# Kernel tuning notes

Measured on AMD Instinct MI355X. Metric: run time of the kernel, lower is better.

The kernel has to match this reference:

```python
import jax, jax.numpy as jnp
import numpy as np

EPS = 1e-6

def _ln(x):
    mu = jnp.mean(x, -1, keepdims=True)
    var = jnp.mean((x - mu) ** 2, -1, keepdims=True)
    return (x - mu) / jnp.sqrt(var + EPS)

def _mha(q_in, k_in, v_in, w, mask, h):
    # w: [4, d, d] = (Wq, Wk, Wv, Wo), stored as [in, out]
    b, sq, d = q_in.shape
    dk = d // h
    q = (q_in @ w[0]).reshape(b, sq, h, dk)
    k = (k_in @ w[1]).reshape(b, k_in.shape[1], h, dk)
    v = (v_in @ w[2]).reshape(b, v_in.shape[1], h, dk)
    scores = jnp.einsum('bqhd,bkhd->bhqk', q, k) / np.sqrt(dk).astype(q.dtype)
    if mask is not None:
        scores = jnp.where(mask, scores, jnp.asarray(-jnp.inf, scores.dtype))
    attn = jax.nn.softmax(scores, -1)
    out = jnp.einsum('bhqk,bkhd->bqhd', attn, v).reshape(b, sq, d)
    return out @ w[3]

def setup_inputs() -> dict:
    B, S, D, V, NL, ML = 8, 256, 1024, 32000, 6, 256
    ks = jax.random.split(jax.random.key(0), 8)
    sc = 0.02
    return {
        'memory': jax.random.normal(ks[0], (B, S, D), jnp.float32),
        'gold_tokens': jax.random.randint(ks[1], (B, ML), 0, V),
        'attn_w': jax.random.normal(ks[2], (NL, 2, 4, D, D), jnp.float32) * sc,
        'ffn_w1': jax.random.normal(ks[3], (NL, D, 4 * D), jnp.float32) * sc,
        'ffn_w2': jax.random.normal(ks[4], (NL, 4 * D, D), jnp.float32) * sc,
        'tok_emb': jax.random.normal(ks[5], (V, D - ML), jnp.float32) * sc,
        'sos': jax.random.normal(ks[6], (D,), jnp.float32),
        'gen_w': jax.random.normal(ks[7], (D, V), jnp.float32) * sc,
    }

def reference(memory, gold_tokens, attn_w, ffn_w1, ffn_w2, tok_emb, sos, gen_w):
    B = memory.shape[0]
    ML = gold_tokens.shape[1]          # max_length == decoder len
    NL = attn_w.shape[0]
    H = 8
    temperature = 1.0
    # embedding: token embed (dim d-ML) concat one-hot position (dim ML)
    dec_input = gold_tokens[:, :-1]                      # [B, ML-1]
    tok = tok_emb[dec_input]                             # [B, ML-1, D-ML]
    pos = jax.nn.one_hot(jnp.arange(ML - 1), ML, dtype=tok.dtype)  # [ML-1, ML]
    pos = jnp.broadcast_to(pos[None], (B, ML - 1, ML))
    emb = jnp.concatenate([tok, pos], -1)                # [B, ML-1, D]
    sos_tok = jnp.broadcast_to(sos[None, None, :], (B, 1, sos.shape[0]))
    x = jnp.concatenate([sos_tok, emb], 1)               # [B, ML, D]
    causal = jnp.tril(jnp.ones((ML, ML), bool))[None, None]  # True = keep
    for l in range(NL):
        h1 = _ln(x)
        x = x + _mha(h1, h1, h1, attn_w[l, 0], causal, H)       # self-attn
        x = x + _mha(_ln(x), memory, memory, attn_w[l, 1], None, H)  # cross-attn (raw memory keys/values)
        h2 = _ln(x)
        x = x + jax.nn.relu(h2 @ ffn_w1[l]) @ ffn_w2[l]
    logits = _ln(x) @ gen_w
    return jax.nn.log_softmax(logits / temperature, -1)
```

## Files before the change

kernel.cpp:

```cpp
#include <hip/hip_runtime.h>
#include <hip/hip_bf16.h>
#include <cstdint>
#include <cstddef>

using bf16 = __hip_bfloat16;
typedef __attribute__((ext_vector_type(8))) short bf16x8;
typedef __attribute__((ext_vector_type(4))) float f32x4;

#define DEV static __device__ __forceinline__

DEV unsigned short f2bf(float f) {
    bf16 h = __float2bfloat16(f);
    return __builtin_bit_cast(unsigned short, h);
}

typedef const __attribute__((address_space(1))) void* as1cv;
typedef __attribute__((address_space(3))) void* as3v;

DEV void load_lds16(const void* g, void* l) {
    __builtin_amdgcn_global_load_lds((as1cv)g, (as3v)l, 16, 0, 0);
}

template<int EPI>
__global__ __launch_bounds__(256)
void gemm_k(const bf16* __restrict__ Ag, const bf16* __restrict__ Bg,
            void* __restrict__ Cg,
            int Mdim, int Ndim, int Kdim,
            int lda, int ldb, int ldc,
            int Hdim, long aZ1, long aZ2, long bZ1, long bZ2,
            long cZ1, long cZ2, float scale,
            const bf16* __restrict__ Ag2, int ySplitA)
{
    __shared__ __align__(16) char lds[65536];

    const int t = threadIdx.x;
    const int wave = t >> 6, lane = t & 63;
    const int wr = wave >> 1, wc = wave & 1;
    const int lo = lane & 15, hi = lane >> 4;

    const int bx2 = blockIdx.x, by2 = blockIdx.y;
    const int m0 = bx2 * 128, n0 = by2 * 128;
    const int z = blockIdx.z;
    const int z1 = z / Hdim, z2 = z - z1 * Hdim;

    const bf16* Abase = (by2 >= ySplitA) ? Ag2 : Ag;
    const bf16* A = Abase + (size_t)z1 * aZ1 + (size_t)z2 * aZ2;
    const bf16* B = Bg + (size_t)z1 * bZ1 + (size_t)z2 * bZ2;

    f32x4 acc[4][4];
#pragma unroll
    for (int m = 0; m < 4; ++m)
#pragma unroll
        for (int n = 0; n < 4; ++n)
            acc[m][n] = f32x4{0.f, 0.f, 0.f, 0.f};

    const int nk = Kdim >> 6;

    auto stage = [&](int kt, int buf) {
        const int k0 = kt << 6;
        char* dA = lds + buf * 32768;
        char* dB = dA + 16384;
#pragma unroll
        for (int i = 0; i < 4; ++i) {
            int u = i * 256 + t;
            int row = u >> 3;
            int cb = (u & 7) ^ (row & 7);
            load_lds16(A + (size_t)(m0 + row) * lda + (k0 + cb * 8),
                       dA + i * 4096 + wave * 1024);
        }
#pragma unroll
        for (int i = 0; i < 4; ++i) {
            int u = i * 256 + t;
            int row = u >> 3;
            int cb = (u & 7) ^ (row & 7);
            load_lds16(B + (size_t)(n0 + row) * ldb + (k0 + cb * 8),
                       dB + i * 4096 + wave * 1024);
        }
    };

    stage(0, 0);
    int cur = 0;
    for (int kt = 0; kt < nk; ++kt) {
        __syncthreads();
        if (kt + 1 < nk) stage(kt + 1, cur ^ 1);
        char* ldsA = lds + cur * 32768;
        char* ldsB = ldsA + 16384;
#pragma unroll
        for (int kk = 0; kk < 2; ++kk) {
            bf16x8 af[4], bfr[4];
#pragma unroll
            for (int m = 0; m < 4; ++m) {
                int row = wr * 64 + m * 16 + lo;
                int cbyte = ((kk << 6) + (hi << 4)) ^ ((row & 7) << 4);
                af[m] = *(const bf16x8*)(ldsA + row * 128 + cbyte);
            }
#pragma unroll
            for (int n = 0; n < 4; ++n) {
                int row = wc * 64 + n * 16 + lo;
                int cbyte = ((kk << 6) + (hi << 4)) ^ ((row & 7) << 4);
                bfr[n] = *(const bf16x8*)(ldsB + row * 128 + cbyte);
            }
#pragma unroll
            for (int m = 0; m < 4; ++m)
#pragma unroll
                for (int n = 0; n < 4; ++n)
                    acc[m][n] = __builtin_amdgcn_mfma_f32_16x16x32_bf16(
                        af[m], bfr[n], acc[m][n], 0, 0, 0);
        }
        cur ^= 1;
    }

    const int rb = hi << 2;
    if (EPI == 0 || EPI == 1) {
        unsigned short* C = (unsigned short*)Cg + (size_t)z1 * cZ1 + (size_t)z2 * cZ2;
#pragma unroll
        for (int m = 0; m < 4; ++m)
#pragma unroll
            for (int n = 0; n < 4; ++n)
#pragma unroll
                for (int r = 0; r < 4; ++r) {
                    int row = m0 + wr * 64 + m * 16 + rb + r;
                    int col = n0 + wc * 64 + n * 16 + lo;
                    float v = acc[m][n][r];
                    if (EPI == 1) v = fmaxf(v, 0.f);
                    C[(size_t)row * ldc + col] = f2bf(v);
                }
    } else if (EPI == 5) {
        float* C = (float*)Cg + (size_t)z1 * cZ1 + (size_t)z2 * cZ2;
#pragma unroll
        for (int m = 0; m < 4; ++m)
#pragma unroll
            for (int n = 0; n < 4; ++n)
#pragma unroll
                for (int r = 0; r < 4; ++r) {
                    int row = m0 + wr * 64 + m * 16 + rb + r;
                    int col = n0 + wc * 64 + n * 16 + lo;
                    atomicAdd(&C[(size_t)row * ldc + col], acc[m][n][r]);
                }
    } else {
        float* C = (float*)Cg + (size_t)z1 * cZ1 + (size_t)z2 * cZ2;
#pragma unroll
        for (int m = 0; m < 4; ++m)
#pragma unroll
            for (int n = 0; n < 4; ++n)
#pragma unroll
                for (int r = 0; r < 4; ++r) {
                    int row = m0 + wr * 64 + m * 16 + rb + r;
                    int col = n0 + wc * 64 + n * 16 + lo;
                    __builtin_nontemporal_store(acc[m][n][r] * scale,
                                                &C[(size_t)row * ldc + col]);
                }
    }
}

template<int CAUSAL>
__global__ __launch_bounds__(256)
void attn_k(const bf16* __restrict__ qkv, const bf16* __restrict__ VT,
            bf16* __restrict__ attno)
{
    __shared__ __align__(16) char ldsK[2][16384];
    __shared__ __align__(16) char ldsP[8192];
    const float SC = 0.088388347648318447f;

    const int t = threadIdx.x, w = t >> 6, lane = t & 63;
    const int lo = lane & 15, hi = lane >> 4;
    const int qb = blockIdx.x, z = blockIdx.y;
    const int b = z >> 3, h = z & 7;
    const int qr0 = qb * 64 + w * 16;

    const unsigned short* Qg = (const unsigned short*)qkv + (size_t)(b * 256) * 3072 + h * 128;
    const unsigned short* Kg = Qg + 1024;
    const unsigned short* VTz = (const unsigned short*)VT + (size_t)z * 32768;

    bf16x8 qf[4];
#pragma unroll
    for (int ks = 0; ks < 4; ++ks)
        qf[ks] = *(const bf16x8*)(Qg + (size_t)(qr0 + lo) * 3072 + ks * 32 + hi * 8);

    f32x4 accO[8];
#pragma unroll
    for (int n2 = 0; n2 < 8; ++n2) accO[n2] = f32x4{0.f, 0.f, 0.f, 0.f};
    float mrun[4], lrun[4];
#pragma unroll
    for (int r = 0; r < 4; ++r) { mrun[r] = -3.0e38f; lrun[r] = 0.f; }

    auto stageK = [&](int kt, int buf) {
#pragma unroll
        for (int i = 0; i < 4; ++i) {
            int u = i * 256 + t;
            int row = u >> 4, j = u & 15;
            int sj = (j & 8) | ((j ^ row) & 7);
            load_lds16(Kg + (size_t)(kt * 64 + row) * 3072 + sj * 8,
                       ldsK[buf] + i * 4096 + w * 1024);
        }
    };

    const int nkt = CAUSAL ? (qb + 1) : 4;
    stageK(0, 0);
    int cur = 0;
    for (int kt = 0; kt < nkt; ++kt) {
        __syncthreads();
        if (kt + 1 < nkt) stageK(kt + 1, cur ^ 1);

        f32x4 s4[4];
#pragma unroll
        for (int n = 0; n < 4; ++n) s4[n] = f32x4{0.f, 0.f, 0.f, 0.f};
#pragma unroll
        for (int ks = 0; ks < 4; ++ks)
#pragma unroll
            for (int n = 0; n < 4; ++n) {
                int kr = n * 16 + lo;
                int c = ks * 4 + hi;
                int sc2 = (c & 8) | ((c ^ (kr & 7)) & 7);
                bf16x8 kf = *(const bf16x8*)(ldsK[cur] + kr * 256 + sc2 * 16);
                s4[n] = __builtin_amdgcn_mfma_f32_16x16x32_bf16(qf[ks], kf, s4[n], 0, 0, 0);
            }

        float sv[4][4];
#pragma unroll
        for (int n = 0; n < 4; ++n)
#pragma unroll
            for (int r = 0; r < 4; ++r) {
                float v = s4[n][r] * SC;
                if (CAUSAL) {
                    int kg = kt * 64 + n * 16 + lo;
                    int qg2 = qb * 64 + w * 16 + hi * 4 + r;
                    if (kg > qg2) v = -3.0e38f;
                }
                sv[n][r] = v;
            }

        float sfv[4];
#pragma unroll
        for (int r = 0; r < 4; ++r) {
            float m2 = fmaxf(fmaxf(sv[0][r], sv[1][r]), fmaxf(sv[2][r], sv[3][r]));
#pragma unroll
            for (int o = 1; o < 16; o <<= 1) m2 = fmaxf(m2, __shfl_xor(m2, o));
            float mn = fmaxf(mrun[r], m2);
            sfv[r] = __expf(mrun[r] - mn);
            mrun[r] = mn;
        }
        float p[4][4], ts[4];
#pragma unroll
        for (int r = 0; r < 4; ++r) ts[r] = 0.f;
#pragma unroll
        for (int n = 0; n < 4; ++n)
#pragma unroll
            for (int r = 0; r < 4; ++r) {
                float e = __expf(sv[n][r] - mrun[r]);
                p[n][r] = e; ts[r] += e;
            }
#pragma unroll
        for (int r = 0; r < 4; ++r) {
            float s2 = ts[r];
#pragma unroll
            for (int o = 1; o < 16; o <<= 1) s2 += __shfl_xor(s2, o);
            lrun[r] = lrun[r] * sfv[r] + s2;
        }
#pragma unroll
        for (int n2 = 0; n2 < 8; ++n2)
#pragma unroll
            for (int r = 0; r < 4; ++r) accO[n2][r] *= sfv[r];

        char* pb = ldsP + w * 2048;
#pragma unroll
        for (int n = 0; n < 4; ++n)
#pragma unroll
            for (int r = 0; r < 4; ++r) {
                int q = hi * 4 + r, k = n * 16 + lo;
                int ch = (k >> 3) ^ (q & 7);
                *(unsigned short*)(pb + q * 128 + ch * 16 + (k & 7) * 2) = f2bf(p[n][r]);
            }

#pragma unroll
        for (int ks2 = 0; ks2 < 2; ++ks2) {
            int c2 = (ks2 * 4 + hi) ^ (lo & 7);
            bf16x8 pa = *(const bf16x8*)(pb + lo * 128 + c2 * 16);
#pragma unroll
            for (int n2 = 0; n2 < 8; ++n2) {
                int d = n2 * 16 + lo;
                bf16x8 vb = *(const bf16x8*)(VTz + (size_t)d * 256 + kt * 64 + ks2 * 32 + hi * 8);
                accO[n2] = __builtin_amdgcn_mfma_f32_16x16x32_bf16(pa, vb, accO[n2], 0, 0, 0);
            }
        }
        cur ^= 1;
    }

    float inv[4];
#pragma unroll
    for (int r = 0; r < 4; ++r) inv[r] = 1.f / lrun[r];
    unsigned short* Og = (unsigned short*)attno;
#pragma unroll
    for (int n2 = 0; n2 < 8; ++n2)
#pragma unroll
        for (int r = 0; r < 4; ++r) {
            int qg2 = qb * 64 + w * 16 + hi * 4 + r;
            int d = n2 * 16 + lo;
            Og[(size_t)(b * 256 + qg2) * 1024 + h * 128 + d] = f2bf(accO[n2][r] * inv[r]);
        }
}

DEV void wconv_tile(const float* __restrict__ W, unsigned short* __restrict__ WT,
                    int K, int N, int k0, int n0, int t, unsigned short* lds)
{
#pragma unroll
    for (int i = 0; i < 16; ++i) {
        int lin = i * 256 + t;
        int r = lin >> 6, c = lin & 63;
        float v = __builtin_nontemporal_load(&W[(size_t)(k0 + r) * N + n0 + c]);
        lds[c * 65 + r] = f2bf(v);
    }
    __syncthreads();
#pragma unroll
    for (int i = 0; i < 16; ++i) {
        int lin = i * 256 + t;
        int r = lin >> 6, c = lin & 63;
        WT[(size_t)(n0 + r) * K + k0 + c] = lds[r * 65 + c];
    }
}

__global__ __launch_bounds__(256)
void wconv_k(const float* __restrict__ W, bf16* __restrict__ WT, int K, int N)
{
    __shared__ unsigned short lds[64 * 65];
    size_t moff = (size_t)blockIdx.z * K * N;
    wconv_tile(W + moff, (unsigned short*)WT + moff, K, N,
               blockIdx.x * 64, blockIdx.y * 64, threadIdx.x, lds);
}

__global__ __launch_bounds__(256)
void wconv3_k(const float* __restrict__ Wa, const float* __restrict__ W1,
              const float* __restrict__ W2, bf16* __restrict__ WTa,
              bf16* __restrict__ WT1, bf16* __restrict__ WT2)
{
    __shared__ unsigned short lds[64 * 65];
    int bid = blockIdx.x, t = threadIdx.x;
    if (bid < 2048) {
        int mat = bid >> 8, r = bid & 255;
        size_t moff = (size_t)mat * 1048576;
        wconv_tile(Wa + moff, (unsigned short*)WTa + moff, 1024, 1024,
                   (r & 15) * 64, (r >> 4) * 64, t, lds);
    } else if (bid < 3072) {
        int idx = bid - 2048;
        wconv_tile(W1, (unsigned short*)WT1, 1024, 4096,
                   (idx & 15) * 64, (idx >> 4) * 64, t, lds);
    } else {
        int idx = bid - 3072;
        wconv_tile(W2, (unsigned short*)WT2, 4096, 1024,
                   (idx & 63) * 64, (idx >> 6) * 64, t, lds);
    }
}

__global__ __launch_bounds__(256)
void f2b_k(const float* __restrict__ in, bf16* __restrict__ out, int n4)
{
    int i = blockIdx.x * 256 + threadIdx.x;
    if (i >= n4) return;
    float4 v = ((const float4*)in)[i];
    ushort4 o;
    o.x = f2bf(v.x); o.y = f2bf(v.y); o.z = f2bf(v.z); o.w = f2bf(v.w);
    ((ushort4*)out)[i] = o;
}

__global__ __launch_bounds__(256)
void embed_k(const float* __restrict__ tok_emb, const int* __restrict__ gold,
             const float* __restrict__ sos, float* __restrict__ x)
{
    int row = blockIdx.x;
    int b = row >> 8, sq = row & 255;
    int c4 = threadIdx.x;
    float4 v;
    if (sq == 0) {
        v = ((const float4*)sos)[c4];
    } else {
        int c = c4 << 2;
        if (c < 768) {
            int tok = gold[b * 256 + sq - 1];
            v = ((const float4*)(tok_emb + (size_t)tok * 768))[c4];
        } else {
            int p = sq - 1;
            v.x = (c + 0 - 768 == p) ? 1.f : 0.f;
            v.y = (c + 1 - 768 == p) ? 1.f : 0.f;
            v.z = (c + 2 - 768 == p) ? 1.f : 0.f;
            v.w = (c + 3 - 768 == p) ? 1.f : 0.f;
        }
    }
    ((float4*)(x + (size_t)row * 1024))[c4] = v;
}

__global__ __launch_bounds__(256)
void ln_k(const float* __restrict__ x, bf16* __restrict__ out)
{
    int row = blockIdx.x;
    const float4* xr = (const float4*)(x + (size_t)row * 1024);
    float4 v = xr[threadIdx.x];
    float s = v.x + v.y + v.z + v.w;
    float ss = v.x * v.x + v.y * v.y + v.z * v.z + v.w * v.w;
    for (int o = 32; o > 0; o >>= 1) { s += __shfl_down(s, o); ss += __shfl_down(ss, o); }
    __shared__ float buf[8];
    int wv = threadIdx.x >> 6;
    if ((threadIdx.x & 63) == 0) { buf[wv] = s; buf[4 + wv] = ss; }
    __syncthreads();
    float S = buf[0] + buf[1] + buf[2] + buf[3];
    float SS = buf[4] + buf[5] + buf[6] + buf[7];
    float mean = S * (1.f / 1024.f);
    float var = SS * (1.f / 1024.f) - mean * mean;
    float rstd = rsqrtf(var + 1e-6f);
    ushort4 o;
    o.x = f2bf((v.x - mean) * rstd);
    o.y = f2bf((v.y - mean) * rstd);
    o.z = f2bf((v.z - mean) * rstd);
    o.w = f2bf((v.w - mean) * rstd);
    ((ushort4*)out)[(size_t)row * 256 + threadIdx.x] = o;
}

__global__ __launch_bounds__(256)
void vtrans_k(const bf16* __restrict__ v, bf16* __restrict__ VT)
{
    __shared__ unsigned short lds[128 * 65];
    int z = blockIdx.y;
    int b = z >> 3, hh = z & 7;
    int sc = blockIdx.x;
    const unsigned short* src = (const unsigned short*)v
        + (size_t)(b * 256 + sc * 64) * 3072 + hh * 128;
    int t = threadIdx.x;
#pragma unroll
    for (int i = 0; i < 32; ++i) {
        int lin = i * 256 + t;
        int sl = lin >> 7, d = lin & 127;
        lds[d * 65 + sl] = src[(size_t)sl * 3072 + d];
    }
    __syncthreads();
    unsigned short* dst = (unsigned short*)VT + (size_t)z * 32768 + sc * 64;
#pragma unroll
    for (int i = 0; i < 32; ++i) {
        int lin = i * 256 + t;
        int d = lin >> 6, sl = lin & 63;
        dst[(size_t)d * 256 + sl] = lds[d * 65 + sl];
    }
}

__global__ __launch_bounds__(512)
void lse1_k(float* __restrict__ out)
{
    const int row = blockIdx.x, t = threadIdx.x;
    f32x4* p = (f32x4*)(out + (size_t)row * 32000);
    f32x4 v[16];
    float m = -3.4e38f, s = 0.f;
#pragma unroll
    for (int i = 0; i < 16; ++i) {
        int idx = i * 512 + t;
        if (idx < 8000) {
            v[i] = __builtin_nontemporal_load(&p[idx]);
            float lm = fmaxf(fmaxf(v[i][0], v[i][1]), fmaxf(v[i][2], v[i][3]));
            if (lm > m) { s *= __expf(m - lm); m = lm; }
            s += __expf(v[i][0] - m) + __expf(v[i][1] - m)
               + __expf(v[i][2] - m) + __expf(v[i][3] - m);
        }
    }
    for (int o = 32; o > 0; o >>= 1) {
        float om = __shfl_down(m, o), os = __shfl_down(s, o);
        float nm = fmaxf(m, om);
        s = s * __expf(m - nm) + os * __expf(om - nm);
        m = nm;
    }
    __shared__ float bm[8], bs[8];
    __shared__ float sL;
    int wv = t >> 6;
    if ((t & 63) == 0) { bm[wv] = m; bs[wv] = s; }
    __syncthreads();
    if (t == 0) {
        float M = -3.4e38f, S = 0.f;
#pragma unroll
        for (int i = 0; i < 8; ++i) {
            float nm = fmaxf(M, bm[i]);
            S = S * __expf(M - nm) + bs[i] * __expf(bm[i] - nm);
            M = nm;
        }
        sL = M + logf(S);
    }
    __syncthreads();
    float L = sL;
#pragma unroll
    for (int i = 0; i < 16; ++i) {
        int idx = i * 512 + t;
        if (idx < 8000) {
            f32x4 w = v[i];
            w[0] -= L; w[1] -= L; w[2] -= L; w[3] -= L;
            __builtin_nontemporal_store(w, &p[idx]);
        }
    }
}

extern "C" void kernel_launch(void* const* d_in, const int* in_sizes, int n_in,
                              void* d_out, int out_size, void* d_ws, size_t ws_size,
                              hipStream_t stream)
{
    (void)in_sizes; (void)n_in; (void)out_size;
    const float* memory  = (const float*)d_in[0];
    const int*   gold    = (const int*)d_in[1];
    const float* attn_w  = (const float*)d_in[2];
    const float* ffn_w1  = (const float*)d_in[3];
    const float* ffn_w2  = (const float*)d_in[4];
    const float* tok_emb = (const float*)d_in[5];
    const float* sos     = (const float*)d_in[6];
    const float* gen_w   = (const float*)d_in[7];
    float* out = (float*)d_out;

    char* ws = (char*)d_ws;
    const size_t o_attnW = 0;
    const size_t o_ffn1W = o_attnW + 16777216;
    const size_t o_ffn2W = o_ffn1W + 8388608;
    const size_t o_qkv   = o_ffn2W + 8388608;
    const size_t o_attno = o_qkv + 12582912;
    const size_t o_tmp   = o_attno + 4194304;
    const size_t o_mem   = o_tmp + 29360128;
    const size_t o_x     = o_mem + 4194304;
    const size_t o_h     = o_x + 8388608;
    const size_t NEEDED  = o_h + 4194304 + 8192;
    if (ws_size < NEEDED) return;

    bf16*  attnWT = (bf16*)(ws + o_attnW);
    bf16*  ffn1WT = (bf16*)(ws + o_ffn1W);
    bf16*  ffn2WT = (bf16*)(ws + o_ffn2W);
    bf16*  qkv    = (bf16*)(ws + o_qkv);
    bf16*  attno  = (bf16*)(ws + o_attno);
    bf16*  VT     = (bf16*)(ws + o_tmp + 25165824);
    bf16*  ffnmid = (bf16*)(ws + o_tmp);
    bf16*  memb   = (bf16*)(ws + o_mem);
    float* x      = (float*)(ws + o_x);
    bf16*  h      = (bf16*)(ws + o_h);
    bf16*  genWT  = (bf16*)(ws + 0);

    const int BIG = 1 << 30;

    f2b_k<<<2048, 256, 0, stream>>>(memory, memb, 2048 * 1024 / 4);
    embed_k<<<2048, 256, 0, stream>>>(tok_emb, gold, sos, x);

    for (int l = 0; l < 6; ++l) {
        wconv3_k<<<4096, 256, 0, stream>>>(attn_w + (size_t)l * 8388608,
            ffn_w1 + (size_t)l * 4194304, ffn_w2 + (size_t)l * 4194304,
            attnWT, ffn1WT, ffn2WT);

        ln_k<<<2048, 256, 0, stream>>>(x, h);
        gemm_k<0><<<dim3(16,24,1), 256, 0, stream>>>(h, attnWT, qkv,
            2048, 3072, 1024, 1024, 1024, 3072, 1, 0,0,0,0,0,0, 0.f, nullptr, BIG);
        vtrans_k<<<dim3(4,64), 256, 0, stream>>>(qkv + 2048, VT);
        attn_k<1><<<dim3(4,64), 256, 0, stream>>>(qkv, VT, attno);
        gemm_k<5><<<dim3(16,8,2), 256, 0, stream>>>(attno, attnWT + 3 * 1048576, x,
            2048, 1024, 512, 1024, 1024, 1024, 2, 0,512, 0,512, 0,0, 0.f, nullptr, BIG);

        ln_k<<<2048, 256, 0, stream>>>(x, h);
        gemm_k<0><<<dim3(16,24,1), 256, 0, stream>>>(h, attnWT + 4 * 1048576, qkv,
            2048, 3072, 1024, 1024, 1024, 3072, 1, 0,0,0,0,0,0, 0.f, memb, 8);
        vtrans_k<<<dim3(4,64), 256, 0, stream>>>(qkv + 2048, VT);
        attn_k<0><<<dim3(4,64), 256, 0, stream>>>(qkv, VT, attno);
        gemm_k<5><<<dim3(16,8,2), 256, 0, stream>>>(attno, attnWT + 7 * 1048576, x,
            2048, 1024, 512, 1024, 1024, 1024, 2, 0,512, 0,512, 0,0, 0.f, nullptr, BIG);

        ln_k<<<2048, 256, 0, stream>>>(x, h);
        gemm_k<1><<<dim3(16,32,1), 256, 0, stream>>>(h, ffn1WT, ffnmid,
            2048, 4096, 1024, 1024, 1024, 4096, 1, 0,0,0,0,0,0, 0.f, nullptr, BIG);
        gemm_k<5><<<dim3(16,8,4), 256, 0, stream>>>(ffnmid, ffn2WT, x,
            2048, 1024, 1024, 4096, 4096, 1024, 4, 0,1024, 0,1024, 0,0, 0.f, nullptr, BIG);
    }

    wconv_k<<<dim3(16,500,1), 256, 0, stream>>>(gen_w, genWT, 1024, 32000);
    ln_k<<<2048, 256, 0, stream>>>(x, h);
    gemm_k<3><<<dim3(16,250,1), 256, 0, stream>>>(h, genWT, out,
        2048, 32000, 1024, 1024, 1024, 32000, 1, 0,0,0,0,0,0, 1.f, nullptr, BIG);
    lse1_k<<<2048, 512, 0, stream>>>(out);
}
```

Before: 1.594 ms.

## Fuse V transpose into attention kernel and stage output through LDS

Removes the separate vtrans_k kernel. The attention kernel now loads V tiles from the qkv buffer into registers, prefetching the next tile during the score computation, and writes them transposed into a swizzled, double-buffered LDS array. The fp32 output GEMM epilogue (EPI 3, the final logits) now stages each tile in padded LDS so it can issue coalesced 16-byte nontemporal stores instead of scattered scalar ones. The output-projection split-K is raised from 2 to 4 slices, which adds atomics in exchange for more parallel blocks. The added LDS use may lower occupancy.

```diff
diff --git a/kernel.cpp b/kernel.cpp
--- a/kernel.cpp
+++ b/kernel.cpp
@@ -31,7 +31,7 @@
             long cZ1, long cZ2, float scale,
             const bf16* __restrict__ Ag2, int ySplitA)
 {
-    __shared__ __align__(16) char lds[65536];
+    __shared__ __align__(16) char lds[67584];
 
     const int t = threadIdx.x;
     const int wave = t >> 6, lane = t & 63;
@@ -139,26 +139,36 @@
                 }
     } else {
         float* C = (float*)Cg + (size_t)z1 * cZ1 + (size_t)z2 * cZ2;
+        float* lf = (float*)lds;
+        __syncthreads();
 #pragma unroll
         for (int m = 0; m < 4; ++m)
 #pragma unroll
             for (int n = 0; n < 4; ++n)
 #pragma unroll
                 for (int r = 0; r < 4; ++r) {
-                    int row = m0 + wr * 64 + m * 16 + rb + r;
-                    int col = n0 + wc * 64 + n * 16 + lo;
-                    __builtin_nontemporal_store(acc[m][n][r] * scale,
-                                                &C[(size_t)row * ldc + col]);
+                    int row = wr * 64 + m * 16 + rb + r;
+                    int col = wc * 64 + n * 16 + lo;
+                    lf[row * 132 + col] = acc[m][n][r] * scale;
                 }
+        __syncthreads();
+#pragma unroll
+        for (int i = 0; i < 16; ++i) {
+            int u = i * 256 + t;
+            int row = u >> 5, c4 = (u & 31) << 2;
+            f32x4 v = *(f32x4*)&lf[row * 132 + c4];
+            __builtin_nontemporal_store(v,
+                (f32x4*)&C[(size_t)(m0 + row) * ldc + n0 + c4]);
+        }
     }
 }
 
 template<int CAUSAL>
 __global__ __launch_bounds__(256)
-void attn_k(const bf16* __restrict__ qkv, const bf16* __restrict__ VT,
-            bf16* __restrict__ attno)
+void attn_k(const bf16* __restrict__ qkv, bf16* __restrict__ attno)
 {
     __shared__ __align__(16) char ldsK[2][16384];
+    __shared__ __align__(16) unsigned short ldsV[2][128][72];
     __shared__ __align__(16) char ldsP[8192];
     const float SC = 0.088388347648318447f;
 
@@ -170,7 +180,7 @@
 
     const unsigned short* Qg = (const unsigned short*)qkv + (size_t)(b * 256) * 3072 + h * 128;
     const unsigned short* Kg = Qg + 1024;
-    const unsigned short* VTz = (const unsigned short*)VT + (size_t)z * 32768;
+    const unsigned short* Vg = Qg + 2048;
 
     bf16x8 qf[4];
 #pragma unroll
@@ -194,9 +204,33 @@
                        ldsK[buf] + i * 4096 + w * 1024);
         }
     };
+    const int sp = t >> 3, dblk = t & 7;
+    auto loadV = [&](int kt, bf16x8* vr) {
+        const unsigned short* src = Vg + (size_t)(kt * 64 + sp * 2) * 3072 + dblk * 16;
+        vr[0] = *(const bf16x8*)(src);
+        vr[1] = *(const bf16x8*)(src + 8);
+        vr[2] = *(const bf16x8*)(src + 3072);
+        vr[3] = *(const bf16x8*)(src + 3072 + 8);
+    };
+    auto writeV = [&](int buf, const bf16x8* vr) {
+        int s0 = sp * 2;
+#pragma unroll
+        for (int half = 0; half < 2; ++half)
+#pragma unroll
+            for (int j = 0; j < 8; ++j) {
+                int d = dblk * 16 + half * 8 + j;
+                int ss = s0 ^ (((d >> 4) & 7) << 3);
+                unsigned int pair = (unsigned short)vr[half][j]
+                                  | ((unsigned int)(unsigned short)vr[2 + half][j] << 16);
+                *(unsigned int*)&ldsV[buf][d][ss] = pair;
+            }
+    };
 
     const int nkt = CAUSAL ? (qb + 1) : 4;
+    bf16x8 vreg[4];
     stageK(0, 0);
+    loadV(0, vreg);
+    writeV(0, vreg);
     int cur = 0;
     for (int kt = 0; kt < nkt; ++kt) {
         __syncthreads();
@@ -215,6 +249,8 @@
                 bf16x8 kf = *(const bf16x8*)(ldsK[cur] + kr * 256 + sc2 * 16);
                 s4[n] = __builtin_amdgcn_mfma_f32_16x16x32_bf16(qf[ks], kf, s4[n], 0, 0, 0);
             }
+
+        if (kt + 1 < nkt) loadV(kt + 1, vreg);
 
         float sv[4][4];
 #pragma unroll
@@ -279,10 +315,13 @@
 #pragma unroll
             for (int n2 = 0; n2 < 8; ++n2) {
                 int d = n2 * 16 + lo;
-                bf16x8 vb = *(const bf16x8*)(VTz + (size_t)d * 256 + kt * 64 + ks2 * 32 + hi * 8);
+                int ss = (ks2 * 32 + hi * 8) ^ (((d >> 4) & 7) << 3);
+                bf16x8 vb = *(const bf16x8*)&ldsV[cur][d][ss];
                 accO[n2] = __builtin_amdgcn_mfma_f32_16x16x32_bf16(pa, vb, accO[n2], 0, 0, 0);
             }
         }
+
+        if (kt + 1 < nkt) writeV(cur ^ 1, vreg);
         cur ^= 1;
     }
 
@@ -414,32 +453,6 @@
     ((ushort4*)out)[(size_t)row * 256 + threadIdx.x] = o;
 }
 
-__global__ __launch_bounds__(256)
-void vtrans_k(const bf16* __restrict__ v, bf16* __restrict__ VT)
-{
-    __shared__ unsigned short lds[128 * 65];
-    int z = blockIdx.y;
-    int b = z >> 3, hh = z & 7;
-    int sc = blockIdx.x;
-    const unsigned short* src = (const unsigned short*)v
-        + (size_t)(b * 256 + sc * 64) * 3072 + hh * 128;
-    int t = threadIdx.x;
-#pragma unroll
-    for (int i = 0; i < 32; ++i) {
-        int lin = i * 256 + t;
-        int sl = lin >> 7, d = lin & 127;
-        lds[d * 65 + sl] = src[(size_t)sl * 3072 + d];
-    }
-    __syncthreads();
-    unsigned short* dst = (unsigned short*)VT + (size_t)z * 32768 + sc * 64;
-#pragma unroll
-    for (int i = 0; i < 32; ++i) {
-        int lin = i * 256 + t;
-        int d = lin >> 6, sl = lin & 63;
-        dst[(size_t)d * 256 + sl] = lds[d * 65 + sl];
-    }
-}
-
 __global__ __launch_bounds__(512)
 void lse1_k(float* __restrict__ out)
 {
@@ -525,7 +538,6 @@
     bf16*  ffn2WT = (bf16*)(ws + o_ffn2W);
     bf16*  qkv    = (bf16*)(ws + o_qkv);
     bf16*  attno  = (bf16*)(ws + o_attno);
-    bf16*  VT     = (bf16*)(ws + o_tmp + 25165824);
     bf16*  ffnmid = (bf16*)(ws + o_tmp);
     bf16*  memb   = (bf16*)(ws + o_mem);
     float* x      = (float*)(ws + o_x);
@@ -545,18 +557,16 @@
         ln_k<<<2048, 256, 0, stream>>>(x, h);
         gemm_k<0><<<dim3(16,24,1), 256, 0, stream>>>(h, attnWT, qkv,
             2048, 3072, 1024, 1024, 1024, 3072, 1, 0,0,0,0,0,0, 0.f, nullptr, BIG);
-        vtrans_k<<<dim3(4,64), 256, 0, stream>>>(qkv + 2048, VT);
-        attn_k<1><<<dim3(4,64), 256, 0, stream>>>(qkv, VT, attno);
-        gemm_k<5><<<dim3(16,8,2), 256, 0, stream>>>(attno, attnWT + 3 * 1048576, x,
-            2048, 1024, 512, 1024, 1024, 1024, 2, 0,512, 0,512, 0,0, 0.f, nullptr, BIG);
+        attn_k<1><<<dim3(4,64), 256, 0, stream>>>(qkv, attno);
+        gemm_k<5><<<dim3(16,8,4), 256, 0, stream>>>(attno, attnWT + 3 * 1048576, x,
+            2048, 1024, 256, 1024, 1024, 1024, 4, 0,256, 0,256, 0,0, 0.f, nullptr, BIG);
 
         ln_k<<<2048, 256, 0, stream>>>(x, h);
         gemm_k<0><<<dim3(16,24,1), 256, 0, stream>>>(h, attnWT + 4 * 1048576, qkv,
             2048, 3072, 1024, 1024, 1024, 3072, 1, 0,0,0,0,0,0, 0.f, memb, 8);
-        vtrans_k<<<dim3(4,64), 256, 0, stream>>>(qkv + 2048, VT);
-        attn_k<0><<<dim3(4,64), 256, 0, stream>>>(qkv, VT, attno);
-        gemm_k<5><<<dim3(16,8,2), 256, 0, stream>>>(attno, attnWT + 7 * 1048576, x,
-            2048, 1024, 512, 1024, 1024, 1024, 2, 0,512, 0,512, 0,0, 0.f, nullptr, BIG);
+        attn_k<0><<<dim3(4,64), 256, 0, stream>>>(qkv, attno);
+        gemm_k<5><<<dim3(16,8,4), 256, 0, stream>>>(attno, attnWT + 7 * 1048576, x,
+            2048, 1024, 256, 1024, 1024, 1024, 4, 0,256, 0,256, 0,0, 0.f, nullptr, BIG);
 
         ln_k<<<2048, 256, 0, stream>>>(x, h);
         gemm_k<1><<<dim3(16,32,1), 256, 0, stream>>>(h, ffn1WT, ffnmid,
```

Result: no change. 1.606 ms (+0.8%).
